# Performance work log

Measured on AMD Instinct MI355X. Metric: run time of the kernel, lower is better.

Reference implementation:

```python
import jax, jax.numpy as jnp
import numpy as np

N = 50000      # n_nodes
E = 800000     # n_edges
IN_NF = 64     # in_node_nf
HID = 128      # hidden_nf
OUT_NF = 64    # out_node_nf
L = 4          # n_layers
EH = HID // 2  # edge MLP hidden width (edge_nf_ratio=2)
C = 1.0        # aggregation scaling constant


def _w(k, shape):
    # fan-in scaled init (matches nn.Linear scale roughly)
    return jax.random.normal(k, shape, dtype=jnp.float32) / np.sqrt(shape[-2]).astype(np.float32)


def setup_inputs() -> dict:
    key = jax.random.key(0)
    ks = jax.random.split(key, 10)
    h = jax.random.normal(ks[0], (N, IN_NF), dtype=jnp.float32)
    edges = jax.random.randint(ks[1], (2, E), 0, N, dtype=jnp.int32)
    return {
        "h": h,
        "edges": edges,
        "W_in": _w(ks[2], (IN_NF, HID)),
        "b_in": jnp.zeros((HID,), jnp.float32),
        # stacked per-layer GCL params, leading dim L
        "eW1": _w(ks[3], (L, 2 * HID, EH)),
        "eb1": jnp.zeros((L, EH), jnp.float32),
        "eW2": _w(ks[4], (L, EH, EH)),
        "eb2": jnp.zeros((L, EH), jnp.float32),
        "nW1": _w(ks[5], (L, HID + EH, HID)),
        "nb1": jnp.zeros((L, HID), jnp.float32),
        "nW2": _w(ks[6], (L, HID, HID)),
        "nb2": jnp.zeros((L, HID), jnp.float32),
        "W_out": _w(ks[7], (HID, OUT_NF)),
        "b_out": jnp.zeros((OUT_NF,), jnp.float32),
    }


def reference(h, edges, W_in, b_in, eW1, eb1, eW2, eb2, nW1, nb1, nW2, nb2, W_out, b_out):
    row, col = edges[0], edges[1]
    h = h @ W_in + b_in  # [N, HID] embedding_in

    def layer(hc, p):
        w1, b1, w2, b2, m1, c1, m2, c2 = p
        # edge model: gather endpoints, concat, 2-layer SiLU MLP
        m = jnp.concatenate([hc[row], hc[col]], axis=1)          # [E, 2*HID]
        m = jax.nn.silu(m @ w1 + b1)                             # [E, EH]
        m = jax.nn.silu(m @ w2 + b2)                             # [E, EH]
        # node model: scatter-sum messages to source nodes, scale by C
        agg = jax.ops.segment_sum(m, row, num_segments=N) * C    # [N, EH]
        z = jnp.concatenate([hc, agg], axis=1)                   # [N, HID+EH]
        z = jax.nn.silu(z @ m1 + c1)
        z = z @ m2 + c2                                          # [N, HID]
        return hc + z, None  # residual=True

    h, _ = jax.lax.scan(layer, h, (eW1, eb1, eW2, eb2, nW1, nb1, nW2, nb2))
    return h @ W_out + b_out  # [N, OUT_NF] embedding_out
```

## Files before the change

kernel.cpp:

```cpp
#include <hip/hip_runtime.h>
#include <hip/hip_bf16.h>
#include <cstdint>
#include <cstddef>

#define N_NODES 50000
#define N_EDGES 800000
#define NR      50048
#define NBKT    196
#define BSH     8
#define BCHUNK  2048
#define CAP     6144

typedef __attribute__((ext_vector_type(8))) short short8;
typedef __attribute__((ext_vector_type(4))) float floatx4;
typedef __attribute__((ext_vector_type(4))) unsigned int uintx4;

__device__ inline float bf2f(unsigned short u) {
    union { unsigned int i; float f; } v; v.i = ((unsigned int)u) << 16; return v.f;
}
__device__ inline unsigned short f2bf(float f) {
    union { float f; unsigned int i; } v; v.f = f;
    unsigned int u = v.i;
    return (unsigned short)((u + 0x7FFFu + ((u >> 16) & 1u)) >> 16);
}
__device__ inline unsigned int f2bf_pk(float a, float b) {
    __hip_bfloat162 h2 = __float22bfloat162_rn(make_float2(a, b));
    return *reinterpret_cast<unsigned int*>(&h2);
}
__device__ inline float2 bf2f2(unsigned int u) {
    union { unsigned int i; float f; } lo, hi;
    lo.i = u << 16;
    hi.i = u & 0xFFFF0000u;
    return make_float2(lo.f, hi.f);
}
__device__ inline float silu_f(float x) {
    float e = __expf(-x);
    return x * __builtin_amdgcn_rcpf(1.0f + e);
}

__device__ inline int block_excl_scan_256(int v, int* buf) {
    int tid = threadIdx.x;
    buf[tid] = v;
    __syncthreads();
    #pragma unroll
    for (int off = 1; off < 256; off <<= 1) {
        int t = (tid >= off) ? buf[tid - off] : 0;
        __syncthreads();
        buf[tid] += t;
        __syncthreads();
    }
    return buf[tid] - v;
}

__device__ inline void pack_std(const float* __restrict__ src,
                                unsigned short* __restrict__ dst,
                                int NOUT, long j) {
    int i = (int)(j & 7);
    long rest = j >> 3;
    int n = (int)(rest % NOUT);
    int kb = (int)(rest / NOUT);
    dst[j] = f2bf(src[(long)(kb * 8 + i) * NOUT + n]);
}

#define NH0   (N_NODES * 64L)
#define SW_IN 8192L
#define SW_OUT 8192L
#define SW1   16384L
#define SE2   4096L
#define SN1   24576L
#define SN2   16384L
#define SB    128L
#define PERL  (SW1 + SE2 + SN1 + SN2 + SB)
#define PACK_TOTAL (NH0 + SW_IN + SW_OUT + 4 * PERL)

__global__ __launch_bounds__(256) void pack_kernel(
    const float* __restrict__ h0, const float* __restrict__ W_in,
    const float* __restrict__ W_out, const float* __restrict__ eW1,
    const float* __restrict__ eb1, const float* __restrict__ eW2,
    const float* __restrict__ nW1, const float* __restrict__ nW2,
    unsigned short* __restrict__ h0bf, unsigned short* __restrict__ Winp,
    unsigned short* __restrict__ Woutp, unsigned short* __restrict__ W1p,
    unsigned short* __restrict__ eW2p, unsigned short* __restrict__ nW1p,
    unsigned short* __restrict__ nW2p, float* __restrict__ biasP)
{
    long idx = (long)blockIdx.x * 256 + threadIdx.x;
    if (idx >= PACK_TOTAL) return;
    long j = idx;
    if (j < NH0) { h0bf[j] = f2bf(h0[j]); return; }
    j -= NH0;
    if (j < SW_IN) { pack_std(W_in, Winp, 128, j); return; }
    j -= SW_IN;
    if (j < SW_OUT) { pack_std(W_out, Woutp, 64, j); return; }
    j -= SW_OUT;
    int l = (int)(j / PERL);
    long r = j % PERL;
    if (r < SW1) {
        int i = (int)(r & 7);
        int n = (int)((r >> 3) & 127);
        int kb = (int)(r >> 10);
        int k = kb * 8 + i;
        const float* w = eW1 + (long)l * 256 * 64;
        float v = (n < 64) ? w[(long)k * 64 + n] : w[(long)(128 + k) * 64 + (n - 64)];
        W1p[(long)l * SW1 + r] = f2bf(v);
        return;
    }
    r -= SW1;
    if (r < SE2) { pack_std(eW2 + (long)l * 4096, eW2p + (long)l * SE2, 64, r); return; }
    r -= SE2;
    if (r < SN1) { pack_std(nW1 + (long)l * 24576, nW1p + (long)l * SN1, 128, r); return; }
    r -= SN1;
    if (r < SN2) { pack_std(nW2 + (long)l * 16384, nW2p + (long)l * SN2, 128, r); return; }
    r -= SN2;
    biasP[(long)l * 128 + r] = (r < 64) ? eb1[(long)l * 64 + r] : 0.0f;
}

__global__ __launch_bounds__(256) void hist_k(const int* __restrict__ erow,
                                              int* __restrict__ countB, int E) {
    __shared__ int c[NBKT];
    for (int i = threadIdx.x; i < NBKT; i += 256) c[i] = 0;
    __syncthreads();
    int j = blockIdx.x * BCHUNK + threadIdx.x;
    #pragma unroll
    for (int i = 0; i < BCHUNK / 256; i++, j += 256)
        if (j < E) atomicAdd(&c[erow[j] >> BSH], 1);
    __syncthreads();
    for (int i = threadIdx.x; i < NBKT; i += 256)
        if (c[i]) atomicAdd(&countB[i], c[i]);
}

__global__ __launch_bounds__(256) void bucket_scan_k(const int* __restrict__ countB,
                                                     int* __restrict__ bucketBase,
                                                     int* __restrict__ bucketCursor) {
    __shared__ int buf[256];
    int tid = threadIdx.x;
    int v = (tid < NBKT) ? countB[tid] : 0;
    int excl = block_excl_scan_256(v, buf);
    if (tid < NBKT) {
        bucketBase[tid] = excl;
        bucketCursor[tid] = excl;
    }
    if (tid == NBKT - 1) bucketBase[NBKT] = excl + v;
}

__global__ __launch_bounds__(256) void bin_k(
    const int* __restrict__ erow, const int* __restrict__ ecol,
    int* __restrict__ bucketCursor, int2* __restrict__ binned, int E)
{
    __shared__ int2 staged[BCHUNK];
    __shared__ int cnt[NBKT];
    __shared__ int binStart[NBKT];
    __shared__ int gbase[NBKT];
    __shared__ int scanbuf[256];
    const int tid = threadIdx.x;
    const int base = blockIdx.x * BCHUNK;
    const int nloc = min(BCHUNK, E - base);

    for (int i = tid; i < NBKT; i += 256) cnt[i] = 0;
    __syncthreads();

    int2 ed[BCHUNK / 256];
    int  bo[BCHUNK / 256];
    #pragma unroll
    for (int i = 0; i < BCHUNK / 256; i++) {
        int jl = i * 256 + tid;
        if (jl < nloc) {
            int j = base + jl;
            int r = erow[j], c = ecol[j];
            ed[i] = make_int2(r, c);
            int b = r >> BSH;
            int off = atomicAdd(&cnt[b], 1);
            bo[i] = (b << 12) | off;
        } else bo[i] = -1;
    }
    __syncthreads();

    int v = (tid < NBKT) ? cnt[tid] : 0;
    int excl = block_excl_scan_256(v, scanbuf);
    if (tid < NBKT) binStart[tid] = excl;
    if (tid < NBKT && v > 0) gbase[tid] = atomicAdd(&bucketCursor[tid], v);
    __syncthreads();

    #pragma unroll
    for (int i = 0; i < BCHUNK / 256; i++) {
        if (bo[i] >= 0)
            staged[binStart[bo[i] >> 12] + (bo[i] & 0xFFF)] = ed[i];
    }
    __syncthreads();

    for (int j = tid; j < nloc; j += 256) {
        int2 e = staged[j];
        int b = e.x >> BSH;
        binned[gbase[b] + (j - binStart[b])] = e;
    }
}

__global__ __launch_bounds__(256) void sort_k(
    const int2* __restrict__ binned, const int* __restrict__ bucketBase,
    int2* __restrict__ eidx)
{
    __shared__ int2 st[CAP];
    __shared__ int cnt[256];
    __shared__ int cur[256];
    __shared__ int scanbuf[256];
    const int b = blockIdx.x;
    const int tid = threadIdx.x;
    const int s0 = bucketBase[b];
    int n = bucketBase[b + 1] - s0;
    if (n > CAP) n = CAP;

    cnt[tid] = 0;
    __syncthreads();
    for (int j = tid; j < n; j += 256) {
        int2 e = binned[s0 + j];
        st[j] = e;
        atomicAdd(&cnt[e.x & 255], 1);
    }
    __syncthreads();
    int excl = block_excl_scan_256(cnt[tid], scanbuf);
    cur[tid] = excl;
    __syncthreads();
    for (int j = tid; j < n; j += 256) {
        int2 e = st[j];
        int pos = atomicAdd(&cur[e.x & 255], 1);
        eidx[s0 + pos] = e;
    }
}

__global__ __launch_bounds__(256) void edge_fused_k(
    const int2* __restrict__ eidx,
    const unsigned short* __restrict__ P,
    const unsigned short* __restrict__ Bp,
    const float* __restrict__ b2, float* __restrict__ agg, int E)
{
    __shared__ float M2s[64 * 68];
    __shared__ int ridS[64];
    __shared__ short segStartS[66];
    __shared__ int nsegS;
    const int tid = threadIdx.x;
    const int wave = tid >> 6;
    const int lane = tid & 63;
    const int lrow = lane & 15;
    const int quad = lane >> 4;
    const int e0 = blockIdx.x * 64;
    const int el = wave * 16 + lrow;
    const int e = e0 + el;

    short8 af0 = {0, 0, 0, 0, 0, 0, 0, 0};
    short8 af1 = af0;
    if (e < E) {
        int2 rc = eidx[e];
        int rr = rc.x, cc = rc.y;
        if (quad == 0) ridS[el] = rr;
        const uintx4* pt = (const uintx4*)(P + (size_t)rr * 128 + quad * 8);
        const uintx4* pb = (const uintx4*)(P + (size_t)cc * 128 + 64 + quad * 8);
        uintx4 t0 = pt[0], t1 = pt[4];
        uintx4 b0 = pb[0], b1 = pb[4];
        const unsigned int* t0u = (const unsigned int*)&t0;
        const unsigned int* t1u = (const unsigned int*)&t1;
        const unsigned int* b0u = (const unsigned int*)&b0;
        const unsigned int* b1u = (const unsigned int*)&b1;
        unsigned int o0[4], o1[4];
        #pragma unroll
        for (int i = 0; i < 4; i++) {
            float2 a0 = bf2f2(t0u[i]), c0 = bf2f2(b0u[i]);
            o0[i] = f2bf_pk(silu_f(a0.x + c0.x), silu_f(a0.y + c0.y));
            float2 a1 = bf2f2(t1u[i]), c1 = bf2f2(b1u[i]);
            o1[i] = f2bf_pk(silu_f(a1.x + c1.x), silu_f(a1.y + c1.y));
        }
        af0 = *(const short8*)o0;
        af1 = *(const short8*)o1;
    } else if (quad == 0) {
        ridS[el] = -1;
    }

    floatx4 acc[4];
    #pragma unroll
    for (int i = 0; i < 4; i++) acc[i] = (floatx4){0, 0, 0, 0};
    #pragma unroll
    for (int nt = 0; nt < 4; nt++) {
        short8 bf0 = *(const short8*)(Bp + (size_t)((0 * 4 + quad) * 64 + nt * 16 + lrow) * 8);
        acc[nt] = __builtin_amdgcn_mfma_f32_16x16x32_bf16(af0, bf0, acc[nt], 0, 0, 0);
        short8 bf1 = *(const short8*)(Bp + (size_t)((1 * 4 + quad) * 64 + nt * 16 + lrow) * 8);
        acc[nt] = __builtin_amdgcn_mfma_f32_16x16x32_bf16(af1, bf1, acc[nt], 0, 0, 0);
    }

    #pragma unroll
    for (int nt = 0; nt < 4; nt++) {
        int n = nt * 16 + lrow;
        float bv = b2[n];
        #pragma unroll
        for (int r = 0; r < 4; r++) {
            int el2 = wave * 16 + quad * 4 + r;
            M2s[el2 * 68 + n] = silu_f(acc[nt][r] + bv);
        }
    }
    __syncthreads();

    if (tid < 64) {
        bool st = (ridS[tid] >= 0) && (tid == 0 || ridS[tid] != ridS[tid - 1]);
        unsigned long long m = __ballot(st);
        if (st) {
            int pos = __popcll(m & ((1ull << tid) - 1));
            segStartS[pos] = (short)tid;
        }
        if (tid == 0) {
            int ns = __popcll(m);
            nsegS = ns;
            int nvalid = E - e0;
            if (nvalid > 64) nvalid = 64;
            segStartS[ns] = (short)nvalid;
        }
    }
    __syncthreads();

    {
        int f = tid & 63;
        int g = tid >> 6;
        int ns = nsegS;
        for (int j = g; j < ns; j += 4) {
            int a = segStartS[j], b = segStartS[j + 1];
            float s = 0.0f;
            for (int el2 = a; el2 < b; el2++) s += M2s[el2 * 68 + f];
            int rv = ridS[a];
            if (j == 0 || j == ns - 1)
                atomicAdd(&agg[(size_t)rv * 64 + f], s);
            else
                agg[(size_t)rv * 64 + f] = s;
        }
    }
}

#define SROW 264
template<int FINAL>
__global__ __launch_bounds__(512) void node_fused_k(
    const unsigned short* __restrict__ hbf, const float* __restrict__ agg,
    const unsigned short* __restrict__ W1, const float* __restrict__ b1,
    const unsigned short* __restrict__ W2, const float* __restrict__ b2,
    const unsigned short* __restrict__ B3, const float* __restrict__ bias3,
    float* __restrict__ hFT, unsigned short* __restrict__ hB,
    unsigned short* __restrict__ Pout, float* __restrict__ outF,
    float* __restrict__ aggZ, int M)
{
    __shared__ unsigned short S[64 * SROW];
    const int tid = threadIdx.x;
    const int m0 = blockIdx.x * 64;
    const int wave = tid >> 6;
    const int lane = tid & 63;
    const int lrow = lane & 15;
    const int quad = lane >> 4;
    const int g = wave >> 1;
    const int h = wave & 1;
    const int row0 = m0 + g * 16 + quad * 4;
    const int elb = g * 16 + quad * 4;

    short8 afa0, afa1;
    {
        const float* ap = agg + (size_t)(m0 + g * 16 + lrow) * 64;
        floatx4 q0 = *(const floatx4*)(ap + quad * 8);
        floatx4 q1 = *(const floatx4*)(ap + quad * 8 + 4);
        floatx4 q2 = *(const floatx4*)(ap + 32 + quad * 8);
        floatx4 q3 = *(const floatx4*)(ap + 32 + quad * 8 + 4);
        unsigned int c0[4] = { f2bf_pk(q0[0], q0[1]), f2bf_pk(q0[2], q0[3]),
                               f2bf_pk(q1[0], q1[1]), f2bf_pk(q1[2], q1[3]) };
        unsigned int c1[4] = { f2bf_pk(q2[0], q2[1]), f2bf_pk(q2[2], q2[3]),
                               f2bf_pk(q3[0], q3[1]), f2bf_pk(q3[2], q3[3]) };
        afa0 = *(const short8*)c0;
        afa1 = *(const short8*)c1;
    }

    floatx4 res4[4];
    #pragma unroll
    for (int j = 0; j < 4; j++) {
        int n = (4 * h + j) * 16 + lrow;
        res4[j] = *(const floatx4*)(hFT + (size_t)n * NR + row0);
    }

    for (int t = tid; t < 64 * 16; t += 512) {
        int rr = t >> 4, c = t & 15;
        int row = m0 + rr;
        uintx4 val = {0, 0, 0, 0};
        if (row < M) val = *(const uintx4*)(hbf + (size_t)row * 128 + c * 8);
        *(uintx4*)(&S[rr * SROW + c * 8]) = val;
    }
    __syncthreads();

    if (!FINAL) {
        floatx4 z = {0, 0, 0, 0};
        for (int t = tid; t < 64 * 16; t += 512) {
            int rr = t >> 4, c = t & 15;
            int row = m0 + rr;
            if (row < M) *(floatx4*)(aggZ + (size_t)row * 64 + c * 4) = z;
        }
    }

    const unsigned short* arow = &S[(g * 16 + lrow) * SROW];

    floatx4 acc[4];
    #pragma unroll
    for (int i = 0; i < 4; i++) acc[i] = (floatx4){0, 0, 0, 0};
    #pragma unroll
    for (int kt = 0; kt < 4; kt++) {
        short8 afrag = *(const short8*)(arow + kt * 32 + quad * 8);
        int kb = kt * 4 + quad;
        #pragma unroll
        for (int j = 0; j < 4; j++) {
            int n = (4 * h + j) * 16 + lrow;
            short8 bfrag = *(const short8*)(W1 + (size_t)(kb * 128 + n) * 8);
            acc[j] = __builtin_amdgcn_mfma_f32_16x16x32_bf16(afrag, bfrag, acc[j], 0, 0, 0);
        }
    }
    #pragma unroll
    for (int j = 0; j < 4; j++) {
        int n = (4 * h + j) * 16 + lrow;
        short8 b4 = *(const short8*)(W1 + (size_t)((16 + quad) * 128 + n) * 8);
        acc[j] = __builtin_amdgcn_mfma_f32_16x16x32_bf16(afa0, b4, acc[j], 0, 0, 0);
        short8 b5 = *(const short8*)(W1 + (size_t)((20 + quad) * 128 + n) * 8);
        acc[j] = __builtin_amdgcn_mfma_f32_16x16x32_bf16(afa1, b5, acc[j], 0, 0, 0);
    }

    #pragma unroll
    for (int j = 0; j < 4; j++) {
        int n = (4 * h + j) * 16 + lrow;
        float bv = b1[n];
        unsigned int p01 = f2bf_pk(silu_f(acc[j][0] + bv), silu_f(acc[j][1] + bv));
        unsigned int p23 = f2bf_pk(silu_f(acc[j][2] + bv), silu_f(acc[j][3] + bv));
        S[(elb + 0) * SROW + 128 + n] = (unsigned short)(p01 & 0xFFFF);
        S[(elb + 1) * SROW + 128 + n] = (unsigned short)(p01 >> 16);
        S[(elb + 2) * SROW + 128 + n] = (unsigned short)(p23 & 0xFFFF);
        S[(elb + 3) * SROW + 128 + n] = (unsigned short)(p23 >> 16);
    }
    __syncthreads();

    floatx4 acc2[4];
    #pragma unroll
    for (int i = 0; i < 4; i++) acc2[i] = (floatx4){0, 0, 0, 0};
    #pragma unroll
    for (int kt = 0; kt < 4; kt++) {
        short8 afrag = *(const short8*)(arow + 128 + kt * 32 + quad * 8);
        int kb = kt * 4 + quad;
        #pragma unroll
        for (int j = 0; j < 4; j++) {
            int n = (4 * h + j) * 16 + lrow;
            short8 bfrag = *(const short8*)(W2 + (size_t)(kb * 128 + n) * 8);
            acc2[j] = __builtin_amdgcn_mfma_f32_16x16x32_bf16(afrag, bfrag, acc2[j], 0, 0, 0);
        }
    }

    #pragma unroll
    for (int j = 0; j < 4; j++) {
        int n = (4 * h + j) * 16 + lrow;
        float bv = b2[n];
        floatx4 v4;
        #pragma unroll
        for (int r = 0; r < 4; r++) v4[r] = acc2[j][r] + bv + res4[j][r];
        unsigned int p01 = f2bf_pk(v4[0], v4[1]);
        unsigned int p23 = f2bf_pk(v4[2], v4[3]);
        S[(elb + 0) * SROW + n] = (unsigned short)(p01 & 0xFFFF);
        S[(elb + 1) * SROW + n] = (unsigned short)(p01 >> 16);
        S[(elb + 2) * SROW + n] = (unsigned short)(p23 & 0xFFFF);
        S[(elb + 3) * SROW + n] = (unsigned short)(p23 >> 16);
        if (!FINAL && row0 < M)
            *(floatx4*)(hFT + (size_t)n * NR + row0) = v4;
    }
    __syncthreads();

    constexpr int NT3 = FINAL ? 2 : 4;
    constexpr int NO3 = FINAL ? 64 : 128;
    floatx4 acc3[NT3];
    #pragma unroll
    for (int i = 0; i < NT3; i++) acc3[i] = (floatx4){0, 0, 0, 0};
    #pragma unroll
    for (int kt = 0; kt < 4; kt++) {
        short8 afrag = *(const short8*)(arow + kt * 32 + quad * 8);
        int kb = kt * 4 + quad;
        #pragma unroll
        for (int j = 0; j < NT3; j++) {
            int n = (NT3 * h + j) * 16 + lrow;
            short8 bfrag = *(const short8*)(B3 + (size_t)(kb * NO3 + n) * 8);
            acc3[j] = __builtin_amdgcn_mfma_f32_16x16x32_bf16(afrag, bfrag, acc3[j], 0, 0, 0);
        }
    }
    #pragma unroll
    for (int j = 0; j < NT3; j++) {
        int n = (NT3 * h + j) * 16 + lrow;
        float bv = bias3[n];
        if (FINAL) {
            #pragma unroll
            for (int r = 0; r < 4; r++)
                ((float*)(&S[(elb + r) * SROW + 128]))[n] = acc3[j][r] + bv;
        } else {
            unsigned int p01 = f2bf_pk(acc3[j][0] + bv, acc3[j][1] + bv);
            unsigned int p23 = f2bf_pk(acc3[j][2] + bv, acc3[j][3] + bv);
            S[(elb + 0) * SROW + 128 + n] = (unsigned short)(p01 & 0xFFFF);
            S[(elb + 1) * SROW + 128 + n] = (unsigned short)(p01 >> 16);
            S[(elb + 2) * SROW + 128 + n] = (unsigned short)(p23 & 0xFFFF);
            S[(elb + 3) * SROW + 128 + n] = (unsigned short)(p23 >> 16);
        }
    }
    __syncthreads();

    if (FINAL) {
        for (int t = tid; t < 64 * 16; t += 512) {
            int rr = t >> 4, c = t & 15;
            int row = m0 + rr;
            if (row < M)
                *(floatx4*)(outF + (size_t)row * 64 + c * 4) =
                    *(const floatx4*)((const float*)(&S[rr * SROW + 128]) + c * 4);
        }
    } else {
        for (int t = tid; t < 64 * 32; t += 512) {
            int rr = t >> 5, c = t & 31;
            int row = m0 + rr;
            if (row < M) {
                if (c < 16)
                    *(uintx4*)(hB + (size_t)row * 128 + c * 8) =
                        *(const uintx4*)(&S[rr * SROW + c * 8]);
                else
                    *(uintx4*)(Pout + (size_t)row * 128 + (c - 16) * 8) =
                        *(const uintx4*)(&S[rr * SROW + 128 + (c - 16) * 8]);
            }
        }
    }
}

#define SROWE 264
__global__ __launch_bounds__(256) void embed_fused_k(
    const unsigned short* __restrict__ h0bf, const unsigned short* __restrict__ Win,
    const float* __restrict__ b_in, const unsigned short* __restrict__ W1,
    const float* __restrict__ biasP, float* __restrict__ hFT,
    unsigned short* __restrict__ hB, unsigned short* __restrict__ Pout, int M)
{
    __shared__ unsigned short S[64 * SROWE];
    const int tid = threadIdx.x;
    const int m0 = blockIdx.x * 64;
    const int wave = tid >> 6;
    const int lane = tid & 63;
    const int lrow = lane & 15;
    const int quad = lane >> 4;
    const int row0 = m0 + wave * 16 + quad * 4;
    const int elb = wave * 16 + quad * 4;

    for (int t = tid; t < 64 * 8; t += 256) {
        int rr = t >> 3, c = t & 7;
        int row = m0 + rr;
        uintx4 val = {0, 0, 0, 0};
        if (row < M) val = *(const uintx4*)(h0bf + (size_t)row * 64 + c * 8);
        *(uintx4*)(&S[rr * SROWE + c * 8]) = val;
    }
    __syncthreads();

    const unsigned short* arow = &S[(wave * 16 + lrow) * SROWE];

    floatx4 acc[8];
    #pragma unroll
    for (int i = 0; i < 8; i++) acc[i] = (floatx4){0, 0, 0, 0};
    #pragma unroll
    for (int kt = 0; kt < 2; kt++) {
        short8 afrag = *(const short8*)(arow + kt * 32 + quad * 8);
        int kb = kt * 4 + quad;
        #pragma unroll
        for (int nt = 0; nt < 8; nt++) {
            short8 bfrag = *(const short8*)(Win + (size_t)(kb * 128 + nt * 16 + lrow) * 8);
            acc[nt] = __builtin_amdgcn_mfma_f32_16x16x32_bf16(afrag, bfrag, acc[nt], 0, 0, 0);
        }
    }

    #pragma unroll
    for (int nt = 0; nt < 8; nt++) {
        int n = nt * 16 + lrow;
        float bv = b_in[n];
        floatx4 v4;
        #pragma unroll
        for (int r = 0; r < 4; r++) v4[r] = acc[nt][r] + bv;
        unsigned int p01 = f2bf_pk(v4[0], v4[1]);
        unsigned int p23 = f2bf_pk(v4[2], v4[3]);
        S[(elb + 0) * SROWE + n] = (unsigned short)(p01 & 0xFFFF);
        S[(elb + 1) * SROWE + n] = (unsigned short)(p01 >> 16);
        S[(elb + 2) * SROWE + n] = (unsigned short)(p23 & 0xFFFF);
        S[(elb + 3) * SROWE + n] = (unsigned short)(p23 >> 16);
        if (row0 < M)
            *(floatx4*)(hFT + (size_t)n * NR + row0) = v4;
    }

    floatx4 acc3[8];
    #pragma unroll
    for (int i = 0; i < 8; i++) acc3[i] = (floatx4){0, 0, 0, 0};
    #pragma unroll
    for (int kt = 0; kt < 4; kt++) {
        short8 afrag = *(const short8*)(arow + kt * 32 + quad * 8);
        int kb = kt * 4 + quad;
        #pragma unroll
        for (int nt = 0; nt < 8; nt++) {
            short8 bfrag = *(const short8*)(W1 + (size_t)(kb * 128 + nt * 16 + lrow) * 8);
            acc3[nt] = __builtin_amdgcn_mfma_f32_16x16x32_bf16(afrag, bfrag, acc3[nt], 0, 0, 0);
        }
    }
    #pragma unroll
    for (int nt = 0; nt < 8; nt++) {
        int n = nt * 16 + lrow;
        float bv = biasP[n];
        unsigned int p01 = f2bf_pk(acc3[nt][0] + bv, acc3[nt][1] + bv);
        unsigned int p23 = f2bf_pk(acc3[nt][2] + bv, acc3[nt][3] + bv);
        S[(elb + 0) * SROWE + 128 + n] = (unsigned short)(p01 & 0xFFFF);
        S[(elb + 1) * SROWE + 128 + n] = (unsigned short)(p01 >> 16);
        S[(elb + 2) * SROWE + 128 + n] = (unsigned short)(p23 & 0xFFFF);
        S[(elb + 3) * SROWE + 128 + n] = (unsigned short)(p23 >> 16);
    }
    __syncthreads();

    for (int t = tid; t < 64 * 32; t += 256) {
        int rr = t / 32, c = t % 32;
        int row = m0 + rr;
        if (row < M) {
            if (c < 16)
                *(uintx4*)(hB + (size_t)row * 128 + c * 8) =
                    *(const uintx4*)(&S[rr * SROWE + c * 8]);
            else
                *(uintx4*)(Pout + (size_t)row * 128 + (c - 16) * 8) =
                    *(const uintx4*)(&S[rr * SROWE + 128 + (c - 16) * 8]);
        }
    }
}

extern "C" void kernel_launch(void* const* d_in, const int* in_sizes, int n_in,
                              void* d_out, int out_size, void* d_ws, size_t ws_size,
                              hipStream_t stream) {
    const float* h0   = (const float*)d_in[0];
    const int*   edges= (const int*)d_in[1];
    const float* W_in = (const float*)d_in[2];
    const float* b_in = (const float*)d_in[3];
    const float* eW1  = (const float*)d_in[4];
    const float* eb1  = (const float*)d_in[5];
    const float* eW2  = (const float*)d_in[6];
    const float* eb2  = (const float*)d_in[7];
    const float* nW1  = (const float*)d_in[8];
    const float* nb1  = (const float*)d_in[9];
    const float* nW2  = (const float*)d_in[10];
    const float* nb2  = (const float*)d_in[11];
    const float* W_out= (const float*)d_in[12];
    const float* b_out= (const float*)d_in[13];
    float* out = (float*)d_out;

    const int E = in_sizes[1] / 2;
    const int* erow = edges;
    const int* ecol = edges + E;

    char* ws = (char*)d_ws;
    unsigned short* hbf  = (unsigned short*)(ws + 0);
    float*          hFT  = (float*)(ws + 12800000);
    unsigned short* P    = (unsigned short*)(ws + 38424576);
    float*          agg  = (float*)(ws + 51224576);
    int2*           binned=(int2*)(ws + 51224576);
    unsigned short* h0bf = (unsigned short*)(ws + 76824576);
    int2*           eidx = (int2*)(ws + 76824576);
    float*          biasP= (float*)(ws + 83224576);
    unsigned short* Winp = (unsigned short*)(ws + 83226624);
    unsigned short* Woutp= (unsigned short*)(ws + 83243008);
    unsigned short* W1p  = (unsigned short*)(ws + 83259392);
    unsigned short* eW2p = (unsigned short*)(ws + 83390464);
    unsigned short* nW1p = (unsigned short*)(ws + 83423232);
    unsigned short* nW2p = (unsigned short*)(ws + 83619840);
    int*            countB=(int*)(ws + 83750912);
    int*            bucketBase=(int*)(ws + 83751936);
    int*            bucketCursor=(int*)(ws + 83752960);

    const int gemm_grid = (N_NODES + 63) / 64;
    const int edge_grid = (E + 63) / 64;
    const int pack_grid = (int)((PACK_TOTAL + 255) / 256);
    const int bin_grid  = (E + BCHUNK - 1) / BCHUNK;

    hipMemsetAsync(countB, 0, NBKT * 4, stream);
    pack_kernel<<<pack_grid, 256, 0, stream>>>(h0, W_in, W_out, eW1, eb1, eW2,
                                               nW1, nW2, h0bf, Winp, Woutp, W1p,
                                               eW2p, nW1p, nW2p, biasP);

    hist_k<<<bin_grid, 256, 0, stream>>>(erow, countB, E);
    bucket_scan_k<<<1, 256, 0, stream>>>(countB, bucketBase, bucketCursor);
    bin_k<<<bin_grid, 256, 0, stream>>>(erow, ecol, bucketCursor, binned, E);

    embed_fused_k<<<gemm_grid, 256, 0, stream>>>(
        h0bf, Winp, b_in, W1p, biasP, hFT, hbf, P, N_NODES);

    sort_k<<<NBKT, 256, 0, stream>>>(binned, bucketBase, eidx);

    hipMemsetAsync(agg, 0, (size_t)N_NODES * 64 * 4, stream);

    for (int l = 0; l < 4; l++) {
        edge_fused_k<<<edge_grid, 256, 0, stream>>>(
            eidx, P, eW2p + (size_t)l * SE2, eb2 + (size_t)l * 64, agg, E);
        if (l < 3) {
            node_fused_k<0><<<gemm_grid, 512, 0, stream>>>(
                hbf, agg, nW1p + (size_t)l * SN1, nb1 + (size_t)l * 128,
                nW2p + (size_t)l * SN2, nb2 + (size_t)l * 128,
                W1p + (size_t)(l + 1) * SW1, biasP + (size_t)(l + 1) * 128,
                hFT, hbf, P, nullptr, agg, N_NODES);
        } else {
            node_fused_k<1><<<gemm_grid, 512, 0, stream>>>(
                hbf, agg, nW1p + (size_t)l * SN1, nb1 + (size_t)l * 128,
                nW2p + (size_t)l * SN2, nb2 + (size_t)l * 128,
                Woutp, b_out, hFT, hbf, nullptr, out, nullptr, N_NODES);
        }
    }
}
```

Baseline: 434.9 us.

## Fold agg zeroing into sort kernel and double edge block to 128 edges

The separate memset of the aggregation buffer is replaced by a grid-stride zero loop at the end of the sort kernel. To allow this, the binned scratch buffer moves to a region that no longer overlaps agg. The edge kernel now processes 128 edges per 512-thread block, with two independent 64-edge halves for segment detection and reduction. This removes one launch and halves the edge grid, at the cost of larger shared memory per block and possibly lower occupancy.

```diff
diff --git a/kernel.cpp b/kernel.cpp
--- a/kernel.cpp
+++ b/kernel.cpp
@@ -196,7 +196,7 @@
 
 __global__ __launch_bounds__(256) void sort_k(
     const int2* __restrict__ binned, const int* __restrict__ bucketBase,
-    int2* __restrict__ eidx)
+    int2* __restrict__ eidx, float* __restrict__ aggZ)
 {
     __shared__ int2 st[CAP];
     __shared__ int cnt[256];
@@ -224,24 +224,29 @@
         int pos = atomicAdd(&cur[e.x & 255], 1);
         eidx[s0 + pos] = e;
     }
-}
-
-__global__ __launch_bounds__(256) void edge_fused_k(
+
+    const int total = N_NODES * 64 / 4;
+    floatx4 z = {0, 0, 0, 0};
+    for (int i = blockIdx.x * 256 + tid; i < total; i += gridDim.x * 256)
+        ((floatx4*)aggZ)[i] = z;
+}
+
+__global__ __launch_bounds__(512) void edge_fused_k(
     const int2* __restrict__ eidx,
     const unsigned short* __restrict__ P,
     const unsigned short* __restrict__ Bp,
     const float* __restrict__ b2, float* __restrict__ agg, int E)
 {
-    __shared__ float M2s[64 * 68];
-    __shared__ int ridS[64];
-    __shared__ short segStartS[66];
-    __shared__ int nsegS;
+    __shared__ float M2s[128 * 68];
+    __shared__ int ridS[128];
+    __shared__ short segStartS[2][66];
+    __shared__ int nsegS[2];
     const int tid = threadIdx.x;
     const int wave = tid >> 6;
     const int lane = tid & 63;
     const int lrow = lane & 15;
     const int quad = lane >> 4;
-    const int e0 = blockIdx.x * 64;
+    const int e0 = blockIdx.x * 128;
     const int el = wave * 16 + lrow;
     const int e = e0 + el;
 
@@ -296,32 +301,39 @@
     }
     __syncthreads();
 
-    if (tid < 64) {
-        bool st = (ridS[tid] >= 0) && (tid == 0 || ridS[tid] != ridS[tid - 1]);
+    if (wave == 0 || wave == 4) {
+        int half = wave >> 2;
+        int base = half * 64;
+        int myel = base + lane;
+        bool st = (ridS[myel] >= 0) &&
+                  (lane == 0 || ridS[myel] != ridS[myel - 1]);
         unsigned long long m = __ballot(st);
         if (st) {
-            int pos = __popcll(m & ((1ull << tid) - 1));
-            segStartS[pos] = (short)tid;
-        }
-        if (tid == 0) {
+            int pos = __popcll(m & ((1ull << lane) - 1));
+            segStartS[half][pos] = (short)lane;
+        }
+        if (lane == 0) {
             int ns = __popcll(m);
-            nsegS = ns;
-            int nvalid = E - e0;
+            nsegS[half] = ns;
+            int nvalid = E - e0 - base;
             if (nvalid > 64) nvalid = 64;
-            segStartS[ns] = (short)nvalid;
+            if (nvalid < 0) nvalid = 0;
+            segStartS[half][ns] = (short)nvalid;
         }
     }
     __syncthreads();
 
     {
-        int f = tid & 63;
-        int g = tid >> 6;
-        int ns = nsegS;
+        int half = wave >> 2;
+        int g = wave & 3;
+        int base = half * 64;
+        int f = lane;
+        int ns = nsegS[half];
         for (int j = g; j < ns; j += 4) {
-            int a = segStartS[j], b = segStartS[j + 1];
+            int a = segStartS[half][j], b = segStartS[half][j + 1];
             float s = 0.0f;
-            for (int el2 = a; el2 < b; el2++) s += M2s[el2 * 68 + f];
-            int rv = ridS[a];
+            for (int el2 = a; el2 < b; el2++) s += M2s[(base + el2) * 68 + f];
+            int rv = ridS[base + a];
             if (j == 0 || j == ns - 1)
                 atomicAdd(&agg[(size_t)rv * 64 + f], s);
             else
@@ -650,7 +662,7 @@
     float*          hFT  = (float*)(ws + 12800000);
     unsigned short* P    = (unsigned short*)(ws + 38424576);
     float*          agg  = (float*)(ws + 51224576);
-    int2*           binned=(int2*)(ws + 51224576);
+    int2*           binned=(int2*)(ws + 64024576);
     unsigned short* h0bf = (unsigned short*)(ws + 76824576);
     int2*           eidx = (int2*)(ws + 76824576);
     float*          biasP= (float*)(ws + 83224576);
@@ -665,7 +677,7 @@
     int*            bucketCursor=(int*)(ws + 83752960);
 
     const int gemm_grid = (N_NODES + 63) / 64;
-    const int edge_grid = (E + 63) / 64;
+    const int edge_grid = (E + 127) / 128;
     const int pack_grid = (int)((PACK_TOTAL + 255) / 256);
     const int bin_grid  = (E + BCHUNK - 1) / BCHUNK;
 
@@ -681,12 +693,10 @@
     embed_fused_k<<<gemm_grid, 256, 0, stream>>>(
         h0bf, Winp, b_in, W1p, biasP, hFT, hbf, P, N_NODES);
 
-    sort_k<<<NBKT, 256, 0, stream>>>(binned, bucketBase, eidx);
-
-    hipMemsetAsync(agg, 0, (size_t)N_NODES * 64 * 4, stream);
+    sort_k<<<NBKT, 256, 0, stream>>>(binned, bucketBase, eidx, agg);
 
     for (int l = 0; l < 4; l++) {
-        edge_fused_k<<<edge_grid, 256, 0, stream>>>(
+        edge_fused_k<<<edge_grid, 512, 0, stream>>>(
             eidx, P, eW2p + (size_t)l * SE2, eb2 + (size_t)l * 64, agg, E);
         if (l < 3) {
             node_fused_k<0><<<gemm_grid, 512, 0, stream>>>(
```

Result: no change. 440.2 us (+1.2%).
